# Kernel optimization log

Hardware: AMD Instinct MI355X
Metric: run time of the kernel (lower is better)

## Reference

```python
import jax, jax.numpy as jnp
import numpy as np

NUM_CLASSES = 80
IGNORE = 0.5
LABEL_SMOOTH = 0.0
MAX_GT = 20
C = 5 + NUM_CLASSES
SIZES = (13, 26, 52)
BS = 64
ANCHORS = jnp.array([
    [[0.0240, 0.0313], [0.0385, 0.0721], [0.0793, 0.0553]],
    [[0.0721, 0.1466], [0.1490, 0.1082], [0.1418, 0.2861]],
    [[0.2788, 0.2163], [0.3750, 0.4760], [0.8966, 0.7837]],
], dtype=jnp.float32)
ANCH_REV = ANCHORS[::-1]  # anchors[[2,1,0]] in the torch code


def bce(p, t):
    p = jnp.clip(p, 1e-7, 1.0 - 1e-7)
    return -t * jnp.log(p) - (1.0 - t) * jnp.log(1.0 - p)


def cal_iou(b1, b2):
    tl = jnp.maximum(b1[..., 0:2] - b1[..., 2:4] / 2, b2[..., 0:2] - b2[..., 2:4] / 2)
    br = jnp.minimum(b1[..., 0:2] + b1[..., 2:4] / 2, b2[..., 0:2] + b2[..., 2:4] / 2)
    wh = jnp.maximum(br - tl, 0.0)
    inter = wh[..., 0] * wh[..., 1]
    union = b1[..., 2] * b1[..., 3] + b2[..., 2] * b2[..., 3] - inter
    return inter / jnp.clip(union, 1e-6)


def _sample_loss(preds, tflat):
    # preds: [N, C] decoded (x,y,w,h,conf,cls...); tflat: [M, C] target grid flattened
    N = preds.shape[0]
    conf_t = tflat[:, 4]
    _, idx = jax.lax.top_k(conf_t, MAX_GT)      # gather up to MAX_GT GT slots
    gts = tflat[idx]                            # [K, C]
    gmask = gts[:, 4]                           # 1.0 for real GT, 0.0 for padding
    iou = cal_iou(gts[:, None, :4], preds[None, :, :4])  # [K, N]
    best = jnp.argmax(iou, axis=-1)             # [K]
    sel = preds[best]                           # [K, C]
    reg = jnp.sum((sel[:, :4] - gts[:, :4]) ** 2, axis=-1) * (2.0 - gts[:, 2] * gts[:, 3])
    loss_reg = jnp.sum(gmask * reg)
    tar_cls = gts[:, 5:] * (1.0 - LABEL_SMOOTH) + LABEL_SMOOTH / NUM_CLASSES
    loss_cls = jnp.sum(gmask[:, None] * bce(sel[:, 5:], tar_cls))
    # noobj mask: zero at best-matched preds (valid GTs only) and at high-IoU preds
    noobj = jnp.ones(N, preds.dtype).at[best].multiply(1.0 - gmask)
    maxiou = jnp.max(iou * gmask[:, None], axis=0)  # [N]
    noobj = noobj * (maxiou < IGNORE).astype(preds.dtype)
    loss_conf = jnp.sum(gmask * bce(sel[:, 4], 1.0)) + jnp.sum(noobj * bce(preds[:, 4], 0.0))
    return loss_reg + loss_conf + loss_cls


def _scale_loss(pred, tgt, l):
    bs, lsz = pred.shape[0], pred.shape[-1]
    p = pred.reshape(bs, 3, C, lsz, lsz).transpose(0, 1, 3, 4, 2)  # [bs,3,h,w,C]
    raw_w, raw_h = p[..., 2], p[..., 3]
    s = jax.nn.sigmoid(p)
    grid = jnp.arange(lsz, dtype=p.dtype)
    x = (grid[None, None, None, :] + s[..., 0]) / lsz
    y = (grid[None, None, :, None] + s[..., 1]) / lsz
    anch = ANCH_REV[l]  # [3,2]
    w = anch[:, 0][None, :, None, None] * jnp.exp(raw_w)
    h = anch[:, 1][None, :, None, None] * jnp.exp(raw_h)
    boxes = jnp.stack([x, y, w, h], axis=-1)
    preds = jnp.concatenate([boxes, s[..., 4:5], s[..., 5:]], axis=-1).reshape(bs, -1, C)
    tflat = tgt.reshape(bs, -1, C)
    return jnp.sum(jax.vmap(_sample_loss)(preds, tflat))


def setup_inputs() -> dict:
    key = jax.random.key(0)
    ks = jax.random.split(key, 6)
    inp = {}
    for i, lsz in enumerate(SIZES):
        inp['pred%d' % i] = jax.random.normal(ks[i], (BS, 3 * C, lsz, lsz), dtype=jnp.float32)
        M = 3 * lsz * lsz
        kb, ki, kc = jax.random.split(ks[3 + i], 3)
        xywh = jax.random.uniform(kb, (BS, MAX_GT, 4), minval=0.05, maxval=0.6, dtype=jnp.float32)
        cls_idx = jax.random.randint(kc, (BS, MAX_GT), 0, NUM_CLASSES)
        entry = jnp.concatenate([xywh, jnp.ones((BS, MAX_GT, 1), jnp.float32),
                                 jax.nn.one_hot(cls_idx, NUM_CLASSES, dtype=jnp.float32)], axis=-1)
        pos = jax.random.randint(ki, (BS, MAX_GT), 0, M)
        tflat = jnp.zeros((BS, M, C), jnp.float32).at[jnp.arange(BS)[:, None], pos].set(entry)
        inp['targets%d' % i] = tflat.reshape(BS, 3, lsz, lsz, C)
    return inp


def reference(pred0, pred1, pred2, targets0, targets1, targets2):
    return (_scale_loss(pred0, targets0, 0)
            + _scale_loss(pred1, targets1, 1)
            + _scale_loss(pred2, targets2, 2))
```

## Files before the change

### kernel.cpp

```cpp
#include <hip/hip_runtime.h>

#define CC 85
#define NC 80
#define MAXGT 20
#define BSZ 64
#define IGNORE_T 0.5f
#define CHUNK 1024
#define NCHMAX 8

#define N0 507
#define N1 2028
#define N2 8112
#define R0 (BSZ*N0)
#define R1 (BSZ*N1)
#define R2 (BSZ*N2)
#define RTOT (R0+R1+R2)

#define CNT_B    (192u*4u)
#define POS_OFF  CNT_B
#define POS_B    (192u*MAXGT*4u)
#define KEY_OFF  (POS_OFF+POS_B)
#define KEY_B    (192u*NCHMAX*MAXGT*8u)
#define NOB_OFF  (KEY_OFF+KEY_B)
#define NOB_B    (192u*NCHMAX*4u)
#define PART_OFF (NOB_OFF+NOB_B)

__constant__ float d_anch[3][3][2] = {
  {{0.2788f,0.2163f},{0.375f,0.476f},{0.8966f,0.7837f}},
  {{0.0721f,0.1466f},{0.149f,0.1082f},{0.1418f,0.2861f}},
  {{0.024f,0.0313f},{0.0385f,0.0721f},{0.0793f,0.0553f}},
};

__device__ __forceinline__ float sigmoidf(float x){ return 1.0f/(1.0f+__expf(-x)); }
__device__ __forceinline__ float bcef(float p, float t){
  p = fminf(fmaxf(p, 1e-7f), 1.0f-1e-7f);
  return -t*__logf(p) - (1.0f-t)*__logf(1.0f-p);
}

template<int N>
__device__ __forceinline__ void scan_one(const float* __restrict__ tgt, int rl,
                                         int s, int* __restrict__ cnt,
                                         int* __restrict__ pos){
  int b = rl / N;
  int n = rl - b*N;
  if (tgt[(size_t)rl*CC + 4] > 0.5f){
    int slot = s*BSZ + b;
    int i = atomicAdd(&cnt[slot], 1);
    if (i < MAXGT) pos[slot*MAXGT + i] = n;
  }
}

__global__ __launch_bounds__(256)
void k_scan(const float* __restrict__ t0, const float* __restrict__ t1,
            const float* __restrict__ t2,
            int* __restrict__ cnt, int* __restrict__ pos){
  int r = blockIdx.x*256 + threadIdx.x;
  if (r < R0)         scan_one<N0>(t0, r,       0, cnt, pos);
  else if (r < R0+R1) scan_one<N1>(t1, r-R0,    1, cnt, pos);
  else if (r < RTOT)  scan_one<N2>(t2, r-R0-R1, 2, cnt, pos);
}

template<int LSZ, int S>
__device__ __forceinline__ void iou_one(const float* __restrict__ pred,
                                        const float* __restrict__ tgt,
                                        int b, int chunk,
                                        const int* __restrict__ cnt,
                                        const int* __restrict__ pos,
                                        unsigned long long* __restrict__ keys,
                                        float* __restrict__ nob){
  constexpr int L2 = LSZ*LSZ, N = 3*L2;
  const int n0 = chunk*CHUNK;
  if (n0 >= N) return;
  const int slot = S*BSZ + b;
  const float* P = pred + (size_t)b*3*CC*L2;
  const float* T = tgt  + (size_t)b*N*CC;
  const int tid = threadIdx.x;
  __shared__ float4 tb[MAXGT];
  __shared__ float  area[MAXGT];
  __shared__ unsigned long long lkey[4][MAXGT];
  __shared__ float  lnob[4];
  if (tid < MAXGT){
    int G = min(cnt[slot], MAXGT);
    float x=0.f,y=0.f,w=0.f,h=0.f;
    if (tid < G){
      const float* r = T + (size_t)pos[slot*MAXGT+tid]*CC;
      x=r[0]; y=r[1]; w=r[2]; h=r[3];
    }
    tb[tid]   = make_float4(x-w*0.5f, y-h*0.5f, x+w*0.5f, y+h*0.5f);
    area[tid] = w*h;
  }
  __syncthreads();
  unsigned long long key[MAXGT];
  #pragma unroll
  for (int g=0; g<MAXGT; g++) key[g]=0ull;
  float noobj = 0.0f;
  const float inv = 1.0f/(float)LSZ;
  const int nend = min(n0+CHUNK, N);
  for (int n = n0+tid; n < nend; n += 256){
    const int a = n/L2, rem = n - a*L2, ii = rem/LSZ, jj = rem - ii*LSZ;
    const float* bp = P + (size_t)a*CC*L2 + rem;
    const float q0=bp[0], q1=bp[L2], q2=bp[2*L2], q3=bp[3*L2], q4=bp[4*L2];
    const float px = ((float)jj + sigmoidf(q0))*inv;
    const float py = ((float)ii + sigmoidf(q1))*inv;
    const float pw = d_anch[S][a][0]*__expf(q2);
    const float ph = d_anch[S][a][1]*__expf(q3);
    const float x0=px-pw*0.5f, x1=px+pw*0.5f, y0=py-ph*0.5f, y1=py+ph*0.5f;
    const float pa = pw*ph;
    float maxi = 0.0f;
    const unsigned long long nin = (unsigned long long)(~(unsigned)n);
    #pragma unroll
    for (int g=0; g<MAXGT; g++){
      const float4 t4 = tb[g];
      const float w = fmaxf(fminf(t4.z,x1) - fmaxf(t4.x,x0), 0.0f);
      const float h = fmaxf(fminf(t4.w,y1) - fmaxf(t4.y,y0), 0.0f);
      const float inter = w*h;
      const float io = inter / fmaxf(area[g]+pa-inter, 1e-6f);
      maxi = fmaxf(maxi, io);
      const unsigned long long k =
        ((unsigned long long)__float_as_uint(io)<<32) | nin;
      if (k > key[g]) key[g] = k;
    }
    if (maxi < IGNORE_T) noobj += bcef(sigmoidf(q4), 0.0f);
  }
  const int wid = tid>>6, lane = tid&63;
  #pragma unroll
  for (int g=0; g<MAXGT; g++){
    unsigned long long k = key[g];
    for (int off=32; off>0; off>>=1){
      const unsigned long long o = __shfl_down(k, off, 64);
      if (o > k) k = o;
    }
    if (lane==0) lkey[wid][g] = k;
  }
  for (int off=32; off>0; off>>=1) noobj += __shfl_down(noobj, off, 64);
  if (lane==0) lnob[wid] = noobj;
  __syncthreads();
  if (tid < MAXGT){
    unsigned long long k = lkey[0][tid];
    #pragma unroll
    for (int w=1; w<4; w++){ const unsigned long long o = lkey[w][tid]; if (o>k) k=o; }
    keys[((size_t)slot*NCHMAX + chunk)*MAXGT + tid] = k;
  }
  if (tid==0) nob[slot*NCHMAX + chunk] = lnob[0]+lnob[1]+lnob[2]+lnob[3];
}

__global__ __launch_bounds__(256, 2)
void k_iou(const float* __restrict__ p0, const float* __restrict__ t0,
           const float* __restrict__ p1, const float* __restrict__ t1,
           const float* __restrict__ p2, const float* __restrict__ t2,
           const int* __restrict__ cnt, const int* __restrict__ pos,
           unsigned long long* __restrict__ keys, float* __restrict__ nob){
  const int chunk = blockIdx.x, b = blockIdx.y, s = blockIdx.z;
  if (s==0)      iou_one<13,0>(p0, t0, b, chunk, cnt, pos, keys, nob);
  else if (s==1) iou_one<26,1>(p1, t1, b, chunk, cnt, pos, keys, nob);
  else           iou_one<52,2>(p2, t2, b, chunk, cnt, pos, keys, nob);
}

template<int LSZ, int S, int NCH>
__device__ __forceinline__ void final_one(const float* __restrict__ pred,
                                          const float* __restrict__ tgt,
                                          int b, int z,
                                          const int* __restrict__ cnt,
                                          const int* __restrict__ pos,
                                          const unsigned long long* __restrict__ keys,
                                          const float* __restrict__ nob,
                                          float* __restrict__ part){
  constexpr int L2 = LSZ*LSZ, N = 3*L2;
  const int slot = S*BSZ + b;
  const float* P = pred + (size_t)b*3*CC*L2;
  const float* T = tgt  + (size_t)b*N*CC;
  const int tid = threadIdx.x;
  __shared__ int bn[MAXGT];
  __shared__ int gp[MAXGT];
  __shared__ float gx[MAXGT], gy[MAXGT], gw[MAXGT], gh[MAXGT];
  __shared__ float4 tb[MAXGT];
  __shared__ float area[MAXGT];
  const int G = min(cnt[slot], MAXGT);
  if (tid < MAXGT){
    unsigned long long k = keys[((size_t)slot*NCHMAX + 0)*MAXGT + tid];
    #pragma unroll
    for (int c=1; c<NCH; c++){
      const unsigned long long o = keys[((size_t)slot*NCHMAX + c)*MAXGT + tid];
      if (o > k) k = o;
    }
    bn[tid] = (int)(~(unsigned)(k & 0xffffffffull));
    float x=0.f,y=0.f,w=0.f,h=0.f; int p=0;
    if (tid < G){
      p = pos[slot*MAXGT + tid];
      const float* r = T + (size_t)p*CC;
      x=r[0]; y=r[1]; w=r[2]; h=r[3];
    }
    gp[tid]=p; gx[tid]=x; gy[tid]=y; gw[tid]=w; gh[tid]=h;
    tb[tid]   = make_float4(x-w*0.5f, y-h*0.5f, x+w*0.5f, y+h*0.5f);
    area[tid] = w*h;
  }
  __syncthreads();
  float loss = 0.0f;
  const float inv = 1.0f/(float)LSZ;
  if (z == 0 && tid < G){
    const int n = bn[tid];
    const int a = n/L2, rem = n - a*L2, i = rem/LSZ, j = rem - i*LSZ;
    const float* bp = P + (size_t)a*CC*L2 + rem;
    const float q0=bp[0], q1=bp[L2], q2=bp[2*L2], q3=bp[3*L2], q4=bp[4*L2];
    const float px = ((float)j + sigmoidf(q0))*inv;
    const float py = ((float)i + sigmoidf(q1))*inv;
    const float pw = d_anch[S][a][0]*__expf(q2);
    const float ph = d_anch[S][a][1]*__expf(q3);
    const float dx=px-gx[tid], dy=py-gy[tid], dw=pw-gw[tid], dh=ph-gh[tid];
    loss += (dx*dx+dy*dy+dw*dw+dh*dh)*(2.0f - gw[tid]*gh[tid]);
    loss += bcef(sigmoidf(q4), 1.0f);
    bool first = true;
    for (int g2=0; g2<tid; g2++) if (bn[g2]==n) first=false;
    if (first){
      const float bx0=px-pw*0.5f, bx1=px+pw*0.5f, by0=py-ph*0.5f, by1=py+ph*0.5f;
      const float parea = pw*ph;
      float maxiou = 0.0f;
      for (int g2=0; g2<MAXGT; g2++){
        const float4 t4 = tb[g2];
        const float w = fmaxf(fminf(t4.z,bx1) - fmaxf(t4.x,bx0), 0.0f);
        const float h = fmaxf(fminf(t4.w,by1) - fmaxf(t4.y,by0), 0.0f);
        const float inter = w*h;
        maxiou = fmaxf(maxiou, inter / fmaxf(area[g2]+parea-inter, 1e-6f));
      }
      if (maxiou < IGNORE_T) loss -= bcef(sigmoidf(q4), 0.0f);
    }
  }
  if (z == 0 && tid == 0){
    #pragma unroll
    for (int c=0; c<NCH; c++) loss += nob[slot*NCHMAX + c];
  }
  for (int idx = z*256 + tid; idx < G*NC; idx += 512){
    const int g = idx/NC, c = idx - g*NC;
    const int n = bn[g];
    const int a = n/L2, rem = n - a*L2;
    const float q  = P[(size_t)a*CC*L2 + (size_t)(5+c)*L2 + rem];
    const float tc = T[(size_t)gp[g]*CC + 5 + c];
    loss += bcef(sigmoidf(q), tc);
  }
  __shared__ float wsum[4];
  for (int off=32; off>0; off>>=1) loss += __shfl_down(loss, off, 64);
  if ((tid&63)==0) wsum[tid>>6] = loss;
  __syncthreads();
  if (tid==0) part[slot*2 + z] = wsum[0]+wsum[1]+wsum[2]+wsum[3];
}

__global__ __launch_bounds__(256)
void k_final(const float* __restrict__ p0, const float* __restrict__ t0,
             const float* __restrict__ p1, const float* __restrict__ t1,
             const float* __restrict__ p2, const float* __restrict__ t2,
             const int* __restrict__ cnt, const int* __restrict__ pos,
             const unsigned long long* __restrict__ keys,
             const float* __restrict__ nob, float* __restrict__ part){
  const int b = blockIdx.x, s = blockIdx.y, z = blockIdx.z;
  if (s==0)      final_one<13,0,1>(p0, t0, b, z, cnt, pos, keys, nob, part);
  else if (s==1) final_one<26,1,2>(p1, t1, b, z, cnt, pos, keys, nob, part);
  else           final_one<52,2,8>(p2, t2, b, z, cnt, pos, keys, nob, part);
}

__global__ __launch_bounds__(384)
void k_sum(const float* __restrict__ part, float* __restrict__ out){
  const int tid = threadIdx.x;
  float v = part[tid];
  for (int off=32; off>0; off>>=1) v += __shfl_down(v, off, 64);
  __shared__ float w[6];
  if ((tid&63)==0) w[tid>>6] = v;
  __syncthreads();
  if (tid==0){
    float s = 0.f;
    #pragma unroll
    for (int i=0; i<6; i++) s += w[i];
    out[0] = s;
  }
}

extern "C" void kernel_launch(void* const* d_in, const int* in_sizes, int n_in,
                              void* d_out, int out_size, void* d_ws, size_t ws_size,
                              hipStream_t stream)
{
  const float* p0 = (const float*)d_in[0];
  const float* t0 = (const float*)d_in[1];
  const float* p1 = (const float*)d_in[2];
  const float* t1 = (const float*)d_in[3];
  const float* p2 = (const float*)d_in[4];
  const float* t2 = (const float*)d_in[5];
  char* ws = (char*)d_ws;
  int*                ws_cnt  = (int*)(ws);
  int*                ws_pos  = (int*)(ws + POS_OFF);
  unsigned long long* ws_keys = (unsigned long long*)(ws + KEY_OFF);
  float*              ws_nob  = (float*)(ws + NOB_OFF);
  float*              ws_part = (float*)(ws + PART_OFF);

  hipMemsetAsync(ws_cnt, 0, CNT_B, stream);

  k_scan <<<(RTOT+255)/256, 256, 0, stream>>>(t0,t1,t2, ws_cnt, ws_pos);
  k_iou  <<<dim3(NCHMAX,BSZ,3), 256, 0, stream>>>(p0,t0,p1,t1,p2,t2,
                                                  ws_cnt, ws_pos, ws_keys, ws_nob);
  k_final<<<dim3(BSZ,3,2), 256, 0, stream>>>(p0,t0,p1,t1,p2,t2,
                                             ws_cnt, ws_pos, ws_keys, ws_nob, ws_part);
  k_sum  <<<1, 384, 0, stream>>>(ws_part, (float*)d_out);
}
```

Before: 402.9 us.

## Stream targets with float4 in scan and fuse final reduction via last-block pattern

```diff
diff --git a/kernel.cpp b/kernel.cpp
--- a/kernel.cpp
+++ b/kernel.cpp
@@ -11,19 +11,22 @@
 #define N0 507
 #define N1 2028
 #define N2 8112
-#define R0 (BSZ*N0)
-#define R1 (BSZ*N1)
-#define R2 (BSZ*N2)
-#define RTOT (R0+R1+R2)
-
-#define CNT_B    (192u*4u)
-#define POS_OFF  CNT_B
+#define RR0 (BSZ*N0)
+#define RR1 (BSZ*N1)
+#define RR2 (BSZ*N2)
+
+#define F0 ((RR0*CC)/4)
+#define F1 ((RR1*CC)/4)
+#define F2 ((RR2*CC)/4)
+
+#define CNT_OFF  0u
+#define DONE_OFF 768u
+#define ZERO_B   1536u
+#define POS_OFF  1536u
 #define POS_B    (192u*MAXGT*4u)
 #define KEY_OFF  (POS_OFF+POS_B)
 #define KEY_B    (192u*NCHMAX*MAXGT*8u)
 #define NOB_OFF  (KEY_OFF+KEY_B)
-#define NOB_B    (192u*NCHMAX*4u)
-#define PART_OFF (NOB_OFF+NOB_B)
 
 __constant__ float d_anch[3][3][2] = {
   {{0.2788f,0.2163f},{0.375f,0.476f},{0.8966f,0.7837f}},
@@ -37,64 +40,87 @@
   return -t*__logf(p) - (1.0f-t)*__logf(1.0f-p);
 }
 
-template<int N>
-__device__ __forceinline__ void scan_one(const float* __restrict__ tgt, int rl,
-                                         int s, int* __restrict__ cnt,
-                                         int* __restrict__ pos){
-  int b = rl / N;
-  int n = rl - b*N;
-  if (tgt[(size_t)rl*CC + 4] > 0.5f){
-    int slot = s*BSZ + b;
-    int i = atomicAdd(&cnt[slot], 1);
-    if (i < MAXGT) pos[slot*MAXGT + i] = n;
+template<int NROWS, int S, int NF>
+__device__ __forceinline__ void scan_stream(const float4* __restrict__ T,
+                                            int* __restrict__ cnt,
+                                            int* __restrict__ pos,
+                                            int gtid, int gstr)
+{
+  for (int i = gtid; i < NF; i += gstr){
+    const float4 v = T[i];
+    const unsigned e = 4u*(unsigned)i;
+    const unsigned q = e / 85u;
+    const unsigned m = e - q*85u;
+    if (m - 1u < 4u){
+      const float c = (m==4u) ? v.x : (m==3u) ? v.y : (m==2u) ? v.z : v.w;
+      if (c > 0.5f){
+        const unsigned b = q / (unsigned)NROWS;
+        const unsigned n = q - b*(unsigned)NROWS;
+        const int slot = S*BSZ + (int)b;
+        const int idx = atomicAdd(&cnt[slot], 1);
+        if (idx < MAXGT) pos[slot*MAXGT + idx] = (int)n;
+      }
+    }
   }
 }
 
 __global__ __launch_bounds__(256)
-void k_scan(const float* __restrict__ t0, const float* __restrict__ t1,
-            const float* __restrict__ t2,
-            int* __restrict__ cnt, int* __restrict__ pos){
-  int r = blockIdx.x*256 + threadIdx.x;
-  if (r < R0)         scan_one<N0>(t0, r,       0, cnt, pos);
-  else if (r < R0+R1) scan_one<N1>(t1, r-R0,    1, cnt, pos);
-  else if (r < RTOT)  scan_one<N2>(t2, r-R0-R1, 2, cnt, pos);
-}
-
-template<int LSZ, int S>
-__device__ __forceinline__ void iou_one(const float* __restrict__ pred,
-                                        const float* __restrict__ tgt,
-                                        int b, int chunk,
-                                        const int* __restrict__ cnt,
-                                        const int* __restrict__ pos,
-                                        unsigned long long* __restrict__ keys,
-                                        float* __restrict__ nob){
+void k_scan(const float4* __restrict__ t0, const float4* __restrict__ t1,
+            const float4* __restrict__ t2,
+            int* __restrict__ cnt, int* __restrict__ pos,
+            float* __restrict__ out)
+{
+  const int gtid = blockIdx.x*256 + threadIdx.x;
+  const int gstr = gridDim.x*256;
+  if (gtid == 0) out[0] = 0.0f;
+  scan_stream<N0,0,F0>(t0, cnt, pos, gtid, gstr);
+  scan_stream<N1,1,F1>(t1, cnt, pos, gtid, gstr);
+  scan_stream<N2,2,F2>(t2, cnt, pos, gtid, gstr);
+}
+
+template<int LSZ, int S, int NCH>
+__device__ __forceinline__ void iou_final_one(
+    const float* __restrict__ pred, const float* __restrict__ tgt,
+    int b, int chunk,
+    const int* __restrict__ cnt, const int* __restrict__ pos,
+    unsigned long long* __restrict__ keys, float* __restrict__ nob,
+    int* __restrict__ done, float* __restrict__ out)
+{
   constexpr int L2 = LSZ*LSZ, N = 3*L2;
-  const int n0 = chunk*CHUNK;
-  if (n0 >= N) return;
+  if (chunk >= NCH) return;
   const int slot = S*BSZ + b;
   const float* P = pred + (size_t)b*3*CC*L2;
   const float* T = tgt  + (size_t)b*N*CC;
   const int tid = threadIdx.x;
   __shared__ float4 tb[MAXGT];
   __shared__ float  area[MAXGT];
+  __shared__ float  gx[MAXGT], gy[MAXGT], gw[MAXGT], gh[MAXGT];
+  __shared__ int    gp[MAXGT];
   __shared__ unsigned long long lkey[4][MAXGT];
   __shared__ float  lnob[4];
+  __shared__ int    bn[MAXGT];
+  __shared__ float  wsum[4];
+  __shared__ int    sLast;
+  const int G = min(cnt[slot], MAXGT);
   if (tid < MAXGT){
-    int G = min(cnt[slot], MAXGT);
-    float x=0.f,y=0.f,w=0.f,h=0.f;
+    float x=0.f,y=0.f,w=0.f,h=0.f; int p=0;
     if (tid < G){
-      const float* r = T + (size_t)pos[slot*MAXGT+tid]*CC;
+      p = pos[slot*MAXGT+tid];
+      const float* r = T + (size_t)p*CC;
       x=r[0]; y=r[1]; w=r[2]; h=r[3];
     }
+    gp[tid]=p; gx[tid]=x; gy[tid]=y; gw[tid]=w; gh[tid]=h;
     tb[tid]   = make_float4(x-w*0.5f, y-h*0.5f, x+w*0.5f, y+h*0.5f);
     area[tid] = w*h;
   }
   __syncthreads();
+
   unsigned long long key[MAXGT];
   #pragma unroll
   for (int g=0; g<MAXGT; g++) key[g]=0ull;
   float noobj = 0.0f;
   const float inv = 1.0f/(float)LSZ;
+  const int n0 = chunk*CHUNK;
   const int nend = min(n0+CHUNK, N);
   for (int n = n0+tid; n < nend; n += 256){
     const int a = n/L2, rem = n - a*L2, ii = rem/LSZ, jj = rem - ii*LSZ;
@@ -142,62 +168,26 @@
     keys[((size_t)slot*NCHMAX + chunk)*MAXGT + tid] = k;
   }
   if (tid==0) nob[slot*NCHMAX + chunk] = lnob[0]+lnob[1]+lnob[2]+lnob[3];
-}
-
-__global__ __launch_bounds__(256, 2)
-void k_iou(const float* __restrict__ p0, const float* __restrict__ t0,
-           const float* __restrict__ p1, const float* __restrict__ t1,
-           const float* __restrict__ p2, const float* __restrict__ t2,
-           const int* __restrict__ cnt, const int* __restrict__ pos,
-           unsigned long long* __restrict__ keys, float* __restrict__ nob){
-  const int chunk = blockIdx.x, b = blockIdx.y, s = blockIdx.z;
-  if (s==0)      iou_one<13,0>(p0, t0, b, chunk, cnt, pos, keys, nob);
-  else if (s==1) iou_one<26,1>(p1, t1, b, chunk, cnt, pos, keys, nob);
-  else           iou_one<52,2>(p2, t2, b, chunk, cnt, pos, keys, nob);
-}
-
-template<int LSZ, int S, int NCH>
-__device__ __forceinline__ void final_one(const float* __restrict__ pred,
-                                          const float* __restrict__ tgt,
-                                          int b, int z,
-                                          const int* __restrict__ cnt,
-                                          const int* __restrict__ pos,
-                                          const unsigned long long* __restrict__ keys,
-                                          const float* __restrict__ nob,
-                                          float* __restrict__ part){
-  constexpr int L2 = LSZ*LSZ, N = 3*L2;
-  const int slot = S*BSZ + b;
-  const float* P = pred + (size_t)b*3*CC*L2;
-  const float* T = tgt  + (size_t)b*N*CC;
-  const int tid = threadIdx.x;
-  __shared__ int bn[MAXGT];
-  __shared__ int gp[MAXGT];
-  __shared__ float gx[MAXGT], gy[MAXGT], gw[MAXGT], gh[MAXGT];
-  __shared__ float4 tb[MAXGT];
-  __shared__ float area[MAXGT];
-  const int G = min(cnt[slot], MAXGT);
+
+  __threadfence();
+  __syncthreads();
+  if (tid==0) sLast = (atomicAdd(&done[slot], 1) == NCH-1) ? 1 : 0;
+  __syncthreads();
+  if (!sLast) return;
+  __threadfence();
+
   if (tid < MAXGT){
-    unsigned long long k = keys[((size_t)slot*NCHMAX + 0)*MAXGT + tid];
+    unsigned long long k = keys[((size_t)slot*NCHMAX)*MAXGT + tid];
     #pragma unroll
     for (int c=1; c<NCH; c++){
       const unsigned long long o = keys[((size_t)slot*NCHMAX + c)*MAXGT + tid];
       if (o > k) k = o;
     }
     bn[tid] = (int)(~(unsigned)(k & 0xffffffffull));
-    float x=0.f,y=0.f,w=0.f,h=0.f; int p=0;
-    if (tid < G){
-      p = pos[slot*MAXGT + tid];
-      const float* r = T + (size_t)p*CC;
-      x=r[0]; y=r[1]; w=r[2]; h=r[3];
-    }
-    gp[tid]=p; gx[tid]=x; gy[tid]=y; gw[tid]=w; gh[tid]=h;
-    tb[tid]   = make_float4(x-w*0.5f, y-h*0.5f, x+w*0.5f, y+h*0.5f);
-    area[tid] = w*h;
   }
   __syncthreads();
   float loss = 0.0f;
-  const float inv = 1.0f/(float)LSZ;
-  if (z == 0 && tid < G){
+  if (tid < G){
     const int n = bn[tid];
     const int a = n/L2, rem = n - a*L2, i = rem/LSZ, j = rem - i*LSZ;
     const float* bp = P + (size_t)a*CC*L2 + rem;
@@ -225,11 +215,11 @@
       if (maxiou < IGNORE_T) loss -= bcef(sigmoidf(q4), 0.0f);
     }
   }
-  if (z == 0 && tid == 0){
+  if (tid==0){
     #pragma unroll
     for (int c=0; c<NCH; c++) loss += nob[slot*NCHMAX + c];
   }
-  for (int idx = z*256 + tid; idx < G*NC; idx += 512){
+  for (int idx = tid; idx < G*NC; idx += 256){
     const int g = idx/NC, c = idx - g*NC;
     const int n = bn[g];
     const int a = n/L2, rem = n - a*L2;
@@ -237,40 +227,24 @@
     const float tc = T[(size_t)gp[g]*CC + 5 + c];
     loss += bcef(sigmoidf(q), tc);
   }
-  __shared__ float wsum[4];
   for (int off=32; off>0; off>>=1) loss += __shfl_down(loss, off, 64);
-  if ((tid&63)==0) wsum[tid>>6] = loss;
-  __syncthreads();
-  if (tid==0) part[slot*2 + z] = wsum[0]+wsum[1]+wsum[2]+wsum[3];
-}
-
-__global__ __launch_bounds__(256)
-void k_final(const float* __restrict__ p0, const float* __restrict__ t0,
-             const float* __restrict__ p1, const float* __restrict__ t1,
-             const float* __restrict__ p2, const float* __restrict__ t2,
-             const int* __restrict__ cnt, const int* __restrict__ pos,
-             const unsigned long long* __restrict__ keys,
-             const float* __restrict__ nob, float* __restrict__ part){
-  const int b = blockIdx.x, s = blockIdx.y, z = blockIdx.z;
-  if (s==0)      final_one<13,0,1>(p0, t0, b, z, cnt, pos, keys, nob, part);
-  else if (s==1) final_one<26,1,2>(p1, t1, b, z, cnt, pos, keys, nob, part);
-  else           final_one<52,2,8>(p2, t2, b, z, cnt, pos, keys, nob, part);
-}
-
-__global__ __launch_bounds__(384)
-void k_sum(const float* __restrict__ part, float* __restrict__ out){
-  const int tid = threadIdx.x;
-  float v = part[tid];
-  for (int off=32; off>0; off>>=1) v += __shfl_down(v, off, 64);
-  __shared__ float w[6];
-  if ((tid&63)==0) w[tid>>6] = v;
-  __syncthreads();
-  if (tid==0){
-    float s = 0.f;
-    #pragma unroll
-    for (int i=0; i<6; i++) s += w[i];
-    out[0] = s;
-  }
+  if (lane==0) wsum[wid] = loss;
+  __syncthreads();
+  if (tid==0) atomicAdd(out, wsum[0]+wsum[1]+wsum[2]+wsum[3]);
+}
+
+__global__ __launch_bounds__(256, 2)
+void k_ioufinal(const float* __restrict__ p0, const float* __restrict__ t0,
+                const float* __restrict__ p1, const float* __restrict__ t1,
+                const float* __restrict__ p2, const float* __restrict__ t2,
+                const int* __restrict__ cnt, const int* __restrict__ pos,
+                unsigned long long* __restrict__ keys, float* __restrict__ nob,
+                int* __restrict__ done, float* __restrict__ out)
+{
+  const int chunk = blockIdx.x, b = blockIdx.y, s = blockIdx.z;
+  if (s==0)      iou_final_one<13,0,1>(p0, t0, b, chunk, cnt, pos, keys, nob, done, out);
+  else if (s==1) iou_final_one<26,1,2>(p1, t1, b, chunk, cnt, pos, keys, nob, done, out);
+  else           iou_final_one<52,2,8>(p2, t2, b, chunk, cnt, pos, keys, nob, done, out);
 }
 
 extern "C" void kernel_launch(void* const* d_in, const int* in_sizes, int n_in,
@@ -284,18 +258,18 @@
   const float* p2 = (const float*)d_in[4];
   const float* t2 = (const float*)d_in[5];
   char* ws = (char*)d_ws;
-  int*                ws_cnt  = (int*)(ws);
+  int*                ws_cnt  = (int*)(ws + CNT_OFF);
+  int*                ws_done = (int*)(ws + DONE_OFF);
   int*                ws_pos  = (int*)(ws + POS_OFF);
   unsigned long long* ws_keys = (unsigned long long*)(ws + KEY_OFF);
   float*              ws_nob  = (float*)(ws + NOB_OFF);
-  float*              ws_part = (float*)(ws + PART_OFF);
-
-  hipMemsetAsync(ws_cnt, 0, CNT_B, stream);
-
-  k_scan <<<(RTOT+255)/256, 256, 0, stream>>>(t0,t1,t2, ws_cnt, ws_pos);
-  k_iou  <<<dim3(NCHMAX,BSZ,3), 256, 0, stream>>>(p0,t0,p1,t1,p2,t2,
-                                                  ws_cnt, ws_pos, ws_keys, ws_nob);
-  k_final<<<dim3(BSZ,3,2), 256, 0, stream>>>(p0,t0,p1,t1,p2,t2,
-                                             ws_cnt, ws_pos, ws_keys, ws_nob, ws_part);
-  k_sum  <<<1, 384, 0, stream>>>(ws_part, (float*)d_out);
-}
+  float*              out     = (float*)d_out;
+
+  hipMemsetAsync(ws, 0, ZERO_B, stream);
+
+  k_scan<<<2048, 256, 0, stream>>>((const float4*)t0, (const float4*)t1,
+                                   (const float4*)t2, ws_cnt, ws_pos, out);
+  k_ioufinal<<<dim3(NCHMAX,BSZ,3), 256, 0, stream>>>(p0,t0,p1,t1,p2,t2,
+                                                     ws_cnt, ws_pos, ws_keys,
+                                                     ws_nob, ws_done, out);
+}
```

After: 624.1 us. 1.55x slower.
